# Kernel optimization log

Measured on AMD Instinct MI355X. Metric: run time of the kernel, lower is better.

## Reference

```python
import jax, jax.numpy as jnp
import numpy as np
import math

F = 32                      # multiplicity per irrep (l0dim = l1dim = l2dim)
NUMBASIS = 8
RCUT = 4.0
BESSEL_END = 5.0
AVG_NEIGHBORS = 25.0
N_NODES = 10000
N_EDGES = 250000
HIDDEN = 64
FEAT = 9 * F                # (1+3+5) components per channel

# uvu tensor-product paths (l_in1, l_edge, l_out) allowed by l/parity selection rules
PATHS = [(0,0,0),(0,1,1),(0,2,2),(1,0,1),(1,1,0),(1,1,2),(1,2,1),(2,0,2),(2,1,1),(2,2,0),(2,2,2)]
_cnt = {}
for (_,_,k) in PATHS:
    _cnt[k] = _cnt.get(k, 0) + 1
# e3nn path weights: irrep_normalization='component', path_normalization='element' (num_elements(uvu)=mul_in2=1)
PATH_W = [math.sqrt((2*k+1) / _cnt[k]) for (_,_,k) in PATHS]

def _su2_cg(j1, j2, j3, m1, m2, m3):
    if m1 + m2 != m3:
        return 0.0
    f = math.factorial
    pref = math.sqrt((2*j3+1) * f(j1+j2-j3) * f(j1-j2+j3) * f(-j1+j2+j3) / f(j1+j2+j3+1))
    pref *= math.sqrt(f(j3+m3) * f(j3-m3) * f(j1-m1) * f(j1+m1) * f(j2-m2) * f(j2+m2))
    s = 0.0
    for k in range(0, j1+j2-j3+1):
        d = [k, j1+j2-j3-k, j1-m1-k, j2+m2-k, j3-j2+m1+k, j3-j1-m2+k]
        if min(d) < 0:
            continue
        s += (-1)**k / (f(d[0])*f(d[1])*f(d[2])*f(d[3])*f(d[4])*f(d[5]))
    return pref * s

def _q(l):
    # complex->real SH change of basis (e3nn convention)
    q = np.zeros((2*l+1, 2*l+1), dtype=np.complex128)
    for m in range(-l, 0):
        q[l+m, l+abs(m)] = 1/math.sqrt(2)
        q[l+m, l-abs(m)] = -1j/math.sqrt(2)
    q[l, l] = 1.0
    for m in range(1, l+1):
        q[l+m, l+abs(m)] = (-1)**m/math.sqrt(2)
        q[l+m, l-abs(m)] = 1j*(-1)**m/math.sqrt(2)
    return (-1j)**l * q

def _w3j(l1, l2, l3):
    C = np.zeros((2*l1+1, 2*l2+1, 2*l3+1))
    for m1 in range(-l1, l1+1):
        for m2 in range(-l2, l2+1):
            for m3 in range(-l3, l3+1):
                C[l1+m1, l2+m2, l3+m3] = _su2_cg(l1, l2, l3, m1, m2, m3)
    W = np.einsum('ij,kl,mn,ikm->jln', _q(l1), _q(l2), np.conj(_q(l3)), C.astype(np.complex128))
    Wr, Wi = np.real(W), np.imag(W)
    W = Wr if np.linalg.norm(Wr) >= np.linalg.norm(Wi) else Wi
    return (W / np.linalg.norm(W)).astype(np.float32)   # unit-Frobenius real 3j, as in e3nn

W3J = {p: _w3j(*p) for p in PATHS}

def _bessel(d):
    # soft_one_hot_linspace(d, 0, 5, 8, basis='bessel', cutoff=True)
    t = d / BESSEL_END
    n = jnp.arange(1, NUMBASIS + 1, dtype=d.dtype)
    safe_t = jnp.where(t > 0, t, 1.0)
    out = math.sqrt(2.0 / BESSEL_END) * jnp.sin(n * jnp.pi * t[:, None]) / safe_t[:, None]
    return out * (((t > 0) & (t < 1)).astype(d.dtype))[:, None]

def _poly_cutoff(d):
    u = d / RCUT                      # p = 6
    env = 1.0 - 6.0 * u**5 + 5.0 * u**6
    return env * (d < RCUT).astype(d.dtype)

def _sph(unit):
    # component-normalized real spherical harmonics l=0,1,2 on unit vectors
    x, y, z = unit[:, 0], unit[:, 1], unit[:, 2]
    y0 = jnp.ones_like(x)[:, None]
    y1 = math.sqrt(3.0) * jnp.stack([y, z, x], axis=-1)
    y2 = jnp.stack([
        math.sqrt(15.0) * x * y,
        math.sqrt(15.0) * y * z,
        (math.sqrt(5.0) / 2.0) * (3.0 * z * z - 1.0),
        math.sqrt(15.0) * x * z,
        (math.sqrt(15.0) / 2.0) * (x * x - y * y),
    ], axis=-1)
    return (y0, y1, y2)

def _forward(nodes, pos, src, dst, w1, b1, w2, b2):
    neighbors = nodes[src]                                    # [E, 9F] gather
    posvec = pos[src] - pos[dst]                              # [E, 3]
    dist = jnp.sqrt(jnp.sum(posvec * posvec, axis=1))         # [E]
    h = jax.nn.silu(_bessel(dist) @ w1 + b1)                  # [E, 64]
    radial = (h @ w2 + b2) * _poly_cutoff(dist)[:, None]      # [E, 11F]
    w = radial.reshape(-1, len(PATHS), F)                     # [E, P, F]
    unit = posvec / jnp.maximum(dist, 1e-12)[:, None]
    ys = _sph(unit)                                           # ([E,1],[E,3],[E,5])
    x0 = neighbors[:, :F].reshape(-1, F, 1)
    x1 = neighbors[:, F:4*F].reshape(-1, F, 3)
    x2 = neighbors[:, 4*F:].reshape(-1, F, 5)
    xs = (x0, x1, x2)
    outs = [0.0, 0.0, 0.0]
    for p, (i, j, k) in enumerate(PATHS):
        Wp = jnp.asarray(W3J[(i, j, k)])                      # [di, dj, dk]
        msg = jnp.einsum('abc,eua,eb,eu->euc', Wp, xs[i], ys[j], w[:, p, :])
        outs[k] = outs[k] + PATH_W[p] * msg
    messages = jnp.concatenate([o.reshape(o.shape[0], -1) for o in outs], axis=1)  # [E, 9F]
    agg = jax.ops.segment_sum(messages, dst, num_segments=N_NODES)
    return agg / math.sqrt(AVG_NEIGHBORS)

def setup_inputs():
    key = jax.random.key(0)
    ks = jax.random.split(key, 6)
    nodes = jax.random.normal(ks[0], (N_NODES, FEAT), dtype=jnp.float32)
    pos = jax.random.normal(ks[1], (N_NODES, 3), dtype=jnp.float32)
    src = jax.random.randint(ks[2], (N_EDGES,), 0, N_NODES)
    dst = jax.random.randint(ks[3], (N_EDGES,), 0, N_NODES)
    w1 = jax.random.normal(ks[4], (NUMBASIS, HIDDEN), dtype=jnp.float32) / math.sqrt(NUMBASIS)
    b1 = jnp.zeros((HIDDEN,), jnp.float32)
    w2 = jax.random.normal(ks[5], (HIDDEN, len(PATHS)*F), dtype=jnp.float32) / math.sqrt(HIDDEN)
    b2 = jnp.zeros((len(PATHS)*F,), jnp.float32)
    return {"nodes": nodes, "pos": pos, "src": src, "dst": dst, "w1": w1, "b1": b1, "w2": w2, "b2": b2}

def reference(nodes, pos, src, dst, w1, b1, w2, b2):
    return _forward(nodes, pos, src, dst, w1, b1, w2, b2)
```

## Files before the change

### kernel.cpp

```cpp
#include <hip/hip_runtime.h>
#include <hip/hip_bf16.h>
#include <cmath>
#include <complex>

#define TPB 256
#define SUBS 8
#define EPG 4
#define NM 115
#define NW3J 363
#define SCAN_T 1024
#define NBUCK 256
#define W2N (64*32*12)

namespace {

double fct(int n){ double r=1; for(int i=2;i<=n;i++) r*=i; return r; }

double su2_cg(int j1,int j2,int j3,int m1,int m2,int m3){
  if(m1+m2!=m3) return 0.0;
  double pref = std::sqrt((2*j3+1)*fct(j1+j2-j3)*fct(j1-j2+j3)*fct(-j1+j2+j3)/fct(j1+j2+j3+1));
  pref *= std::sqrt(fct(j3+m3)*fct(j3-m3)*fct(j1-m1)*fct(j1+m1)*fct(j2-m2)*fct(j2+m2));
  double s=0;
  for(int k=0;k<=j1+j2-j3;k++){
    int d0=k, d1=j1+j2-j3-k, d2=j1-m1-k, d3=j2+m2-k, d4=j3-j2+m1+k, d5=j3-j1-m2+k;
    if(d0<0||d1<0||d2<0||d3<0||d4<0||d5<0) continue;
    double t = 1.0/(fct(d0)*fct(d1)*fct(d2)*fct(d3)*fct(d4)*fct(d5));
    s += (k&1)? -t : t;
  }
  return pref*s;
}

typedef std::complex<double> cd;

void qmat(int l, cd q[5][5]){
  for(int i=0;i<5;i++) for(int j=0;j<5;j++) q[i][j] = cd(0,0);
  const double is2 = 1.0/std::sqrt(2.0);
  for(int m=-l;m<0;m++){ q[l+m][l-m] = cd(is2,0); q[l+m][l+m] = cd(0,-is2); }
  q[l][l] = cd(1,0);
  for(int m=1;m<=l;m++){ double sg = (m&1)? -1.0: 1.0; q[l+m][l+m] = cd(sg*is2,0); q[l+m][l-m] = cd(0, sg*is2); }
  cd ph(1,0), mi(0,-1);
  for(int t=0;t<l;t++) ph *= mi;
  for(int i=0;i<5;i++) for(int j=0;j<5;j++) q[i][j] *= ph;
}

void w3j_calc(int l1,int l2,int l3,double* out){
  int n1=2*l1+1,n2=2*l2+1,n3=2*l3+1;
  double C[5][5][5] = {};
  for(int m1=-l1;m1<=l1;m1++)for(int m2=-l2;m2<=l2;m2++)for(int m3=-l3;m3<=l3;m3++)
    C[l1+m1][l2+m2][l3+m3] = su2_cg(l1,l2,l3,m1,m2,m3);
  cd q1[5][5], q2[5][5], q3[5][5];
  qmat(l1,q1); qmat(l2,q2); qmat(l3,q3);
  double wr[125], wi[125];
  double nr=0, ni=0;
  for(int a=0;a<n1;a++)for(int b=0;b<n2;b++)for(int c=0;c<n3;c++){
    cd s(0,0);
    for(int i=0;i<n1;i++)for(int k=0;k<n2;k++)for(int m=0;m<n3;m++)
      s += q1[i][a]*q2[k][b]*std::conj(q3[m][c])*C[i][k][m];
    int idx = (a*n2+b)*n3+c;
    wr[idx]=s.real(); wi[idx]=s.imag();
    nr += s.real()*s.real(); ni += s.imag()*s.imag();
  }
  bool useR = std::sqrt(nr) >= std::sqrt(ni);
  double nn = std::sqrt(useR? nr: ni);
  for(int q=0;q<n1*n2*n3;q++) out[q] = (useR? wr[q]: wi[q])/nn;
}

struct UploadArg {
  float w3j[NW3J];
  unsigned int meta[NM];
};

UploadArg g_upload;

struct BuildInit {
  BuildInit(){
    const int P[11][3] = {{0,0,0},{0,1,1},{0,2,2},{1,0,1},{1,1,0},{1,1,2},
                          {1,2,1},{2,0,2},{2,1,1},{2,2,0},{2,2,2}};
    const int cnt[3] = {3,4,4};
    const int AO[3] = {0,1,4};
    int off = 0, t = 0;
    for(int p=0;p<11;p++){
      int i=P[p][0], j=P[p][1], k=P[p][2];
      int na=2*i+1, nb=2*j+1, nc=2*k+1;
      double W[125];
      w3j_calc(i,j,k,W);
      double pw = std::sqrt((2.0*k+1.0)/(double)cnt[k]);
      for(int q=0;q<na*nb*nc;q++) g_upload.w3j[off+q] = (float)(W[q]*pw);
      for(int a=0;a<na;a++)
        for(int c=0;c<nc;c++)
          g_upload.meta[t++] = (unsigned)((off + a*nb*nc + c) | (nc<<10) | (nb<<14) | (AO[j]<<18));
      off += na*nb*nc;
    }
  }
};
BuildInit g_build_init;

}


__global__ void count_repack_kernel(const int* __restrict__ dst, int* __restrict__ counts,
                                    const float* __restrict__ w2,
                                    unsigned short* __restrict__ w2b, int E){
  int i = blockIdx.x*blockDim.x + threadIdx.x;
  if(i < W2N){
    int pp = i % 12;
    int u  = (i/12) % 32;
    int j  = i / (12*32);
    unsigned short o = 0;
    if(pp < 11){
      unsigned ub = __float_as_uint(w2[j*352 + pp*32 + u]);
      ub = (ub + 0x7fffu + ((ub>>16)&1u)) >> 16;
      o = (unsigned short)ub;
    }
    w2b[i] = o;
  }
  if(i < E) atomicAdd(&counts[dst[i]], 1);
}

__global__ __launch_bounds__(SCAN_T) void megascan_kernel(const int* __restrict__ counts,
                                                          int* __restrict__ off,
                                                          int* __restrict__ cursor,
                                                          int* __restrict__ bcur, int NN){
  __shared__ int part[SCAN_T];
  __shared__ int lh[NBUCK];
  int t = threadIdx.x;
  if(t < NBUCK) lh[t] = 0;
  __syncthreads();
  int C = (NN + SCAN_T - 1)/SCAN_T;
  int base = t*C;
  int lim = min(base+C, NN);
  int s = 0;
  for(int i=base;i<lim;i++){
    int c = counts[i];
    s += c;
    atomicAdd(&lh[min(c, NBUCK-1)], 1);
  }
  part[t] = s;
  __syncthreads();
  for(int d=1; d<SCAN_T; d<<=1){
    int v = (t>=d)? part[t-d] : 0;
    __syncthreads();
    part[t] += v;
    __syncthreads();
  }
  int run = part[t] - s;
  for(int i=base;i<lim;i++){ off[i]=run; cursor[i]=run; run += counts[i]; }
  if(t == SCAN_T-1) off[NN] = part[t];
  __syncthreads();
  if(t == 0){
    int r = 0;
    for(int b=0;b<NBUCK;b++){ bcur[b] = r; r += lh[b]; }
  }
}

__global__ void scatter_kernel(const int* __restrict__ dst, const int* __restrict__ counts,
                               int* __restrict__ cursor, int* __restrict__ bcur,
                               int* __restrict__ node_order, int* __restrict__ eid,
                               int NN, int E){
  int i = blockIdx.x*blockDim.x + threadIdx.x;
  if(i < NN){
    int p = atomicAdd(&bcur[min(counts[i], NBUCK-1)], 1);
    node_order[p] = i;
  }
  if(i < E){
    int p = atomicAdd(&cursor[dst[i]], 1);
    eid[p] = i;
  }
}


__device__ __forceinline__ void up2(unsigned w, float& lo, float& hi){
  lo = __uint_as_float(w << 16);
  hi = __uint_as_float(w & 0xffff0000u);
}

__global__ __launch_bounds__(TPB) void node_kernel(
    const float* __restrict__ nodes,
    const float* __restrict__ pos,
    const int* __restrict__ src,
    const int* __restrict__ node_order,
    const int* __restrict__ off,
    const int* __restrict__ eid,
    const unsigned short* __restrict__ w2b,
    const float* __restrict__ w1,
    const float* __restrict__ b1,
    const float* __restrict__ b2,
    float* __restrict__ outp,
    int NN,
    UploadArg up)
{
  __shared__ float s_w3j[NW3J];
  __shared__ float s_w1[512];
  __shared__ float s_b1[64];
  __shared__ unsigned short s_w2[W2N];
  __shared__ float s_y[SUBS][EPG][12];
  __shared__ float s_h[SUBS][64][EPG];
  __shared__ float s_M[SUBS][EPG][NM+1];

  const int tid = threadIdx.x;
  const int u = tid & 31;
  const int sub = tid >> 5;

  for(int t = tid; t < NW3J; t += TPB) s_w3j[t] = up.w3j[t];
  for(int t = tid; t < 512; t += TPB)  s_w1[t]  = w1[t];
  if(tid < 64) s_b1[tid] = b1[tid];
  {
    const uint4* g4 = (const uint4*)w2b;
    uint4* s4 = (uint4*)s_w2;
    #pragma unroll
    for(int t=0; t<12; t++) s4[tid + t*TPB] = g4[tid + t*TPB];
  }
  __syncthreads();

  const int nidx = blockIdx.x*SUBS + sub;
  const bool active = nidx < NN;
  const int node = active ? node_order[nidx] : 0;
  const int start = off[node];
  const int deg = active ? (off[node+1] - start) : 0;

  float b2r[11];
  #pragma unroll
  for(int p=0;p<11;p++) b2r[p] = b2[p*32+u];
  const float dpx = pos[node*3+0], dpy = pos[node*3+1], dpz = pos[node*3+2];

  float accv[9];
  #pragma unroll
  for(int q=0;q<9;q++) accv[q] = 0.0f;

  constexpr int PI_[11]   = {0,0,0,1,1,1,1,2,2,2,2};
  constexpr int PK_[11]   = {0,1,2,1,0,2,1,2,1,0,2};
  constexpr int TOFF_[11] = {0,1,4,9,18,21,36,45,70,85,90};
  constexpr int AO_[3]    = {0,1,4};

  const int nch = (deg + EPG - 1)/EPG;

  for(int ch=0; ch<nch; ch++){
    float bes[EPG][8];
    float cut[EPG];
    int vsrc[EPG];
    bool valid[EPG];

    #pragma unroll
    for(int e=0;e<EPG;e++){
      int ei = ch*EPG + e;
      bool v = (ei < deg);
      valid[e] = v;
      int eg = v ? eid[start + ei] : 0;
      int se = v ? src[eg] : node;
      vsrc[e] = se;
      float px = pos[se*3+0] - dpx;
      float py = pos[se*3+1] - dpy;
      float pz = pos[se*3+2] - dpz;
      float d2 = px*px + py*py + pz*pz;
      float d = sqrtf(d2);
      float inv = 1.0f / fmaxf(d, 1e-12f);
      float x = px*inv, y = py*inv, z = pz*inv;
      float yv[9];
      yv[0] = 1.0f;
      yv[1] = 1.7320508075688772f*y;
      yv[2] = 1.7320508075688772f*z;
      yv[3] = 1.7320508075688772f*x;
      yv[4] = 3.872983346207417f*x*y;
      yv[5] = 3.872983346207417f*y*z;
      yv[6] = 1.118033988749895f*(3.0f*z*z - 1.0f);
      yv[7] = 3.872983346207417f*x*z;
      yv[8] = 1.9364916731037085f*(x*x - y*y);
      #pragma unroll
      for(int q=0;q<9;q++) s_y[sub][e][q] = yv[q];
      float tt = d * 0.2f;
      float st = (tt > 0.0f) ? tt : 1.0f;
      float msk = (tt > 0.0f && tt < 1.0f) ? 1.0f : 0.0f;
      float ang = 3.14159265358979323846f * tt;
      float s1 = __sinf(ang), c1 = __cosf(ang);
      float kk = 0.6324555320336759f * msk / st;
      float c2 = 2.0f*c1;
      float sp = 0.0f, sc = s1;
      bes[e][0] = kk*s1;
      #pragma unroll
      for(int n=1;n<8;n++){ float sn = c2*sc - sp; sp = sc; sc = sn; bes[e][n] = kk*sn; }
      float uu = d*0.25f;
      float u2 = uu*uu;
      float u5 = u2*u2*uu;
      float env = 1.0f - 6.0f*u5 + 5.0f*u5*uu;
      cut[e] = (d < 4.0f) ? env : 0.0f;
    }

    #pragma unroll
    for(int half=0; half<2; half++){
      int j = u + 32*half;
      float hb = s_b1[j];
      float hh[EPG];
      #pragma unroll
      for(int e=0;e<EPG;e++){
        float a = hb;
        #pragma unroll
        for(int k=0;k<8;k++) a += bes[e][k]*s_w1[k*64+j];
        float sg = 1.0f/(1.0f + __expf(-a));
        hh[e] = a*sg;
      }
      float4 hv; hv.x = hh[0]; hv.y = hh[1]; hv.z = hh[2]; hv.w = hh[3];
      *(float4*)(&s_h[sub][j][0]) = hv;
    }

    #pragma unroll
    for(int w=0; w<4; w++){
      int t = u + 32*w;
      if(t < NM){
        unsigned int md = up.meta[t];
        int woff = md & 1023;
        int nc   = (md>>10) & 15;
        int nb   = (md>>14) & 15;
        int boff = (md>>18) & 15;
        #pragma unroll
        for(int e=0;e<EPG;e++){
          float s = 0.0f;
          for(int b=0;b<nb;b++) s += s_w3j[woff + b*nc] * s_y[sub][e][boff + b];
          s_M[sub][e][t] = s;
        }
      }
    }

    float wacc[EPG][11];
    #pragma unroll
    for(int e=0;e<EPG;e++)
      #pragma unroll
      for(int p=0;p<11;p++) wacc[e][p] = 0.0f;
    for(int j=0;j<64;j++){
      float4 hv = *(const float4*)(&s_h[sub][j][0]);
      const unsigned short* wrow = &s_w2[(j*32+u)*12];
      uint2 wa = *(const uint2*)(wrow);
      uint2 wb = *(const uint2*)(wrow+4);
      uint2 wc = *(const uint2*)(wrow+8);
      float sw[12];
      up2(wa.x, sw[0], sw[1]);  up2(wa.y, sw[2], sw[3]);
      up2(wb.x, sw[4], sw[5]);  up2(wb.y, sw[6], sw[7]);
      up2(wc.x, sw[8], sw[9]);  up2(wc.y, sw[10], sw[11]);
      float hh[4]; hh[0]=hv.x; hh[1]=hv.y; hh[2]=hv.z; hh[3]=hv.w;
      #pragma unroll
      for(int e=0;e<EPG;e++)
        #pragma unroll
        for(int p=0;p<11;p++) wacc[e][p] += hh[e]*sw[p];
    }

    #pragma unroll
    for(int e=0;e<EPG;e++){
      if(!valid[e]) continue;
      const float* nr = nodes + (long)vsrc[e]*288;
      float xv[9];
      xv[0] = nr[u];
      #pragma unroll
      for(int c=0;c<3;c++) xv[1+c] = nr[32 + u*3 + c];
      #pragma unroll
      for(int c=0;c<5;c++) xv[4+c] = nr[128 + u*5 + c];
      float wr[11];
      #pragma unroll
      for(int p=0;p<11;p++) wr[p] = (wacc[e][p] + b2r[p]) * cut[e];
      const float* Me = &s_M[sub][e][0];
      #pragma unroll
      for(int p=0;p<11;p++){
        const int na = 2*PI_[p]+1;
        const int nc = 2*PK_[p]+1;
        const float wv = wr[p];
        #pragma unroll
        for(int a=0;a<na;a++){
          float xw = xv[AO_[PI_[p]]+a] * wv;
          #pragma unroll
          for(int c=0;c<nc;c++){
            accv[AO_[PK_[p]]+c] += xw * Me[TOFF_[p] + a*nc + c];
          }
        }
      }
    }
  }

  if(active){
    float* ob = outp + (long)node*288;
    ob[u] = 0.2f*accv[0];
    #pragma unroll
    for(int c=0;c<3;c++) ob[32 + u*3 + c] = 0.2f*accv[1+c];
    #pragma unroll
    for(int c=0;c<5;c++) ob[128 + u*5 + c] = 0.2f*accv[4+c];
  }
}


extern "C" void kernel_launch(void* const* d_in, const int* in_sizes, int n_in,
                              void* d_out, int out_size, void* d_ws, size_t ws_size,
                              hipStream_t stream) {
  const float* nodes = (const float*)d_in[0];
  const float* pos   = (const float*)d_in[1];
  const int* src = (const int*)d_in[2];
  const int* dst = (const int*)d_in[3];
  const float* w1 = (const float*)d_in[4];
  const float* b1 = (const float*)d_in[5];
  const float* w2 = (const float*)d_in[6];
  const float* b2 = (const float*)d_in[7];

  const int E  = in_sizes[2];
  const int NN = in_sizes[0] / 288;
  float* outp = (float*)d_out;

  unsigned short* w2b = (unsigned short*)d_ws;
  int* counts     = (int*)(w2b + W2N);
  int* offp       = counts + NN;
  int* cursor     = offp + NN + 1;
  int* bcur       = cursor + NN;
  int* node_order = bcur + NBUCK;
  int* eid        = node_order + NN;

  hipMemsetAsync(counts, 0, (size_t)NN*sizeof(int), stream);

  int g1 = (max(E, W2N) + 255)/256;
  count_repack_kernel<<<g1, 256, 0, stream>>>(dst, counts, w2, w2b, E);
  megascan_kernel<<<1, SCAN_T, 0, stream>>>(counts, offp, cursor, bcur, NN);
  int g2 = (max(E, NN) + 255)/256;
  scatter_kernel<<<g2, 256, 0, stream>>>(dst, counts, cursor, bcur, node_order, eid, NN, E);

  int nblocks = (NN + SUBS - 1)/SUBS;
  node_kernel<<<nblocks, TPB, 0, stream>>>(nodes, pos, src, node_order, offp, eid,
                                           w2b, w1, b1, b2, outp, NN, g_upload);
}
```

Baseline: 544.7 us.

## Compute edge radial MLP second layer with bf16 MFMA, one wave per node

Moves the hidden-to-path-weight matmul (64x352 per edge) onto MFMA 16x16x32 bf16 instructions, splitting hidden activations into high and low bf16 parts to keep near-fp32 accuracy. W2 is stored transposed in LDS with an XOR swizzle to avoid bank conflicts. Work is reorganized so each 64-lane wave handles one node with 16 edges per chunk, and lanes split channels and edges before a cross-lane shuffle reduction. The cost is more LDS per block, more complex indexing, and wasted work on nodes whose degree is low relative to the 16-edge chunk.

New measurement: 561.0 us. +3.0%, slower.

```diff
diff --git a/kernel.cpp b/kernel.cpp
--- a/kernel.cpp
+++ b/kernel.cpp
@@ -1,16 +1,19 @@
 #include <hip/hip_runtime.h>
-#include <hip/hip_bf16.h>
 #include <cmath>
 #include <complex>
 
-#define TPB 256
-#define SUBS 8
-#define EPG 4
+#define TPB 512
+#define NPB 8
+#define EPG 16
 #define NM 115
 #define NW3J 363
 #define SCAN_T 1024
 #define NBUCK 256
-#define W2N (64*32*12)
+#define W2N (352*64)
+
+typedef __attribute__((ext_vector_type(8))) short bf16x8;
+typedef __attribute__((ext_vector_type(4))) float f32x4;
+typedef uint4 __attribute__((may_alias)) uint4a;
 
 namespace {
 
@@ -100,19 +103,13 @@
 
 __global__ void count_repack_kernel(const int* __restrict__ dst, int* __restrict__ counts,
                                     const float* __restrict__ w2,
-                                    unsigned short* __restrict__ w2b, int E){
+                                    unsigned short* __restrict__ w2t, int E){
   int i = blockIdx.x*blockDim.x + threadIdx.x;
   if(i < W2N){
-    int pp = i % 12;
-    int u  = (i/12) % 32;
-    int j  = i / (12*32);
-    unsigned short o = 0;
-    if(pp < 11){
-      unsigned ub = __float_as_uint(w2[j*352 + pp*32 + u]);
-      ub = (ub + 0x7fffu + ((ub>>16)&1u)) >> 16;
-      o = (unsigned short)ub;
-    }
-    w2b[i] = o;
+    int n = i >> 6, k = i & 63;
+    unsigned ub = __float_as_uint(w2[k*352 + n]);
+    ub = (ub + 0x7fffu + ((ub>>16)&1u)) >> 16;
+    w2t[i] = (unsigned short)ub;
   }
   if(i < E) atomicAdd(&counts[dst[i]], 1);
 }
@@ -169,19 +166,14 @@
 }
 
 
-__device__ __forceinline__ void up2(unsigned w, float& lo, float& hi){
-  lo = __uint_as_float(w << 16);
-  hi = __uint_as_float(w & 0xffff0000u);
-}
-
-__global__ __launch_bounds__(TPB) void node_kernel(
+__global__ __launch_bounds__(TPB, 2) void node_kernel(
     const float* __restrict__ nodes,
     const float* __restrict__ pos,
     const int* __restrict__ src,
     const int* __restrict__ node_order,
     const int* __restrict__ off,
     const int* __restrict__ eid,
-    const unsigned short* __restrict__ w2b,
+    const unsigned short* __restrict__ w2t,
     const float* __restrict__ w1,
     const float* __restrict__ b1,
     const float* __restrict__ b2,
@@ -189,72 +181,84 @@
     int NN,
     UploadArg up)
 {
-  __shared__ float s_w3j[NW3J];
+  __shared__ __align__(16) unsigned short s_w2t[W2N];
   __shared__ float s_w1[512];
   __shared__ float s_b1[64];
-  __shared__ unsigned short s_w2[W2N];
-  __shared__ float s_y[SUBS][EPG][12];
-  __shared__ float s_h[SUBS][64][EPG];
-  __shared__ float s_M[SUBS][EPG][NM+1];
+  __shared__ float s_b2[352];
+  __shared__ float s_w3j[NW3J];
+  __shared__ unsigned int s_meta[NM];
+  __shared__ float s_M[NPB][16][117];
+  __shared__ float s_y[NPB][16][12];
+  __shared__ float s_cut[NPB][16];
+  __shared__ int   s_srcv[NPB][16];
 
   const int tid = threadIdx.x;
-  const int u = tid & 31;
-  const int sub = tid >> 5;
-
-  for(int t = tid; t < NW3J; t += TPB) s_w3j[t] = up.w3j[t];
-  for(int t = tid; t < 512; t += TPB)  s_w1[t]  = w1[t];
+
+  for(int t=tid; t<NW3J; t+=TPB) s_w3j[t] = up.w3j[t];
+  for(int t=tid; t<NM;   t+=TPB) s_meta[t] = up.meta[t];
+  for(int t=tid; t<512;  t+=TPB) s_w1[t]  = w1[t];
   if(tid < 64) s_b1[tid] = b1[tid];
+  if(tid >= 64 && tid < 64+352) s_b2[tid-64] = b2[tid-64];
   {
-    const uint4* g4 = (const uint4*)w2b;
-    uint4* s4 = (uint4*)s_w2;
-    #pragma unroll
-    for(int t=0; t<12; t++) s4[tid + t*TPB] = g4[tid + t*TPB];
+    const uint4* g4 = (const uint4*)w2t;
+    uint4a* s4 = (uint4a*)s_w2t;
+    for(int c=tid; c<W2N/8; c+=TPB) s4[c ^ ((c>>3)&7)] = g4[c];
   }
   __syncthreads();
 
-  const int nidx = blockIdx.x*SUBS + sub;
+  const int lane = tid & 63;
+  const int wv   = tid >> 6;
+  const int q    = lane >> 4;
+  const int le   = lane & 15;
+  const int swz  = (le & 7) << 4;
+
+  const int nidx = blockIdx.x*NPB + wv;
   const bool active = nidx < NN;
   const int node = active ? node_order[nidx] : 0;
   const int start = off[node];
   const int deg = active ? (off[node+1] - start) : 0;
 
-  float b2r[11];
-  #pragma unroll
-  for(int p=0;p<11;p++) b2r[p] = b2[p*32+u];
   const float dpx = pos[node*3+0], dpy = pos[node*3+1], dpz = pos[node*3+2];
-
-  float accv[9];
-  #pragma unroll
-  for(int q=0;q<9;q++) accv[q] = 0.0f;
 
   constexpr int PI_[11]   = {0,0,0,1,1,1,1,2,2,2,2};
   constexpr int PK_[11]   = {0,1,2,1,0,2,1,2,1,0,2};
   constexpr int TOFF_[11] = {0,1,4,9,18,21,36,45,70,85,90};
   constexpr int AO_[3]    = {0,1,4};
 
+  float accv[2][9];
+  #pragma unroll
+  for(int uh=0; uh<2; uh++)
+    #pragma unroll
+    for(int m=0; m<9; m++) accv[uh][m] = 0.0f;
+
+  const char* wtb = (const char*)s_w2t;
   const int nch = (deg + EPG - 1)/EPG;
 
   for(int ch=0; ch<nch; ch++){
-    float bes[EPG][8];
-    float cut[EPG];
-    int vsrc[EPG];
-    bool valid[EPG];
-
-    #pragma unroll
-    for(int e=0;e<EPG;e++){
-      int ei = ch*EPG + e;
-      bool v = (ei < deg);
-      valid[e] = v;
-      int eg = v ? eid[start + ei] : 0;
-      int se = v ? src[eg] : node;
-      vsrc[e] = se;
-      float px = pos[se*3+0] - dpx;
-      float py = pos[se*3+1] - dpy;
-      float pz = pos[se*3+2] - dpz;
-      float d2 = px*px + py*py + pz*pz;
-      float d = sqrtf(d2);
-      float inv = 1.0f / fmaxf(d, 1e-12f);
-      float x = px*inv, y = py*inv, z = pz*inv;
+    const int ei = ch*EPG + le;
+    const bool valid = ei < deg;
+    const int eg = valid ? eid[start + ei] : 0;
+    const int se = valid ? src[eg] : node;
+    const float px = pos[se*3+0]-dpx, py = pos[se*3+1]-dpy, pz = pos[se*3+2]-dpz;
+    const float d2 = px*px + py*py + pz*pz;
+    const float d  = sqrtf(d2);
+    const float inv = 1.0f / fmaxf(d, 1e-12f);
+    const float x = px*inv, y = py*inv, z = pz*inv;
+
+    float bes[8];
+    {
+      float tt = d * 0.2f;
+      float st = (tt > 0.0f) ? tt : 1.0f;
+      float msk = (tt > 0.0f && tt < 1.0f) ? 1.0f : 0.0f;
+      float ang = 3.14159265358979323846f * tt;
+      float s1 = __sinf(ang), c1 = __cosf(ang);
+      float kk = 0.6324555320336759f * msk / st;
+      float c2 = 2.0f*c1, sp = 0.0f, sc = s1;
+      bes[0] = kk*s1;
+      #pragma unroll
+      for(int n=1;n<8;n++){ float sn = c2*sc - sp; sp = sc; sc = sn; bes[n] = kk*sn; }
+    }
+    if(q == 0){
       float yv[9];
       yv[0] = 1.0f;
       yv[1] = 1.7320508075688772f*y;
@@ -266,120 +270,114 @@
       yv[7] = 3.872983346207417f*x*z;
       yv[8] = 1.9364916731037085f*(x*x - y*y);
       #pragma unroll
-      for(int q=0;q<9;q++) s_y[sub][e][q] = yv[q];
-      float tt = d * 0.2f;
-      float st = (tt > 0.0f) ? tt : 1.0f;
-      float msk = (tt > 0.0f && tt < 1.0f) ? 1.0f : 0.0f;
-      float ang = 3.14159265358979323846f * tt;
-      float s1 = __sinf(ang), c1 = __cosf(ang);
-      float kk = 0.6324555320336759f * msk / st;
-      float c2 = 2.0f*c1;
-      float sp = 0.0f, sc = s1;
-      bes[e][0] = kk*s1;
-      #pragma unroll
-      for(int n=1;n<8;n++){ float sn = c2*sc - sp; sp = sc; sc = sn; bes[e][n] = kk*sn; }
-      float uu = d*0.25f;
-      float u2 = uu*uu;
-      float u5 = u2*u2*uu;
+      for(int m=0;m<9;m++) s_y[wv][le][m] = yv[m];
+      float uu = d*0.25f, u2 = uu*uu, u5 = u2*u2*uu;
       float env = 1.0f - 6.0f*u5 + 5.0f*u5*uu;
-      cut[e] = (d < 4.0f) ? env : 0.0f;
-    }
-
-    #pragma unroll
-    for(int half=0; half<2; half++){
-      int j = u + 32*half;
-      float hb = s_b1[j];
-      float hh[EPG];
-      #pragma unroll
-      for(int e=0;e<EPG;e++){
-        float a = hb;
+      s_cut[wv][le] = (valid && d < 4.0f) ? env : 0.0f;
+      s_srcv[wv][le] = se;
+    }
+
+    bf16x8 Ah0, Al0, Ah1, Al1;
+    #pragma unroll
+    for(int e=0; e<8; e++){
+      #pragma unroll
+      for(int half=0; half<2; half++){
+        const int j = half*32 + q*8 + e;
+        float a = s_b1[j];
         #pragma unroll
-        for(int k=0;k<8;k++) a += bes[e][k]*s_w1[k*64+j];
+        for(int k=0;k<8;k++) a += bes[k]*s_w1[k*64+j];
         float sg = 1.0f/(1.0f + __expf(-a));
-        hh[e] = a*sg;
+        float h = a*sg;
+        unsigned ub = __float_as_uint(h);
+        unsigned hb = (ub + 0x7fffu + ((ub>>16)&1u)) >> 16;
+        float hif = __uint_as_float(hb << 16);
+        unsigned ul = __float_as_uint(h - hif);
+        unsigned lb = (ul + 0x7fffu + ((ul>>16)&1u)) >> 16;
+        if(half == 0){ Ah0[e] = (short)hb; Al0[e] = (short)lb; }
+        else         { Ah1[e] = (short)hb; Al1[e] = (short)lb; }
       }
-      float4 hv; hv.x = hh[0]; hv.y = hh[1]; hv.z = hh[2]; hv.w = hh[3];
-      *(float4*)(&s_h[sub][j][0]) = hv;
-    }
-
-    #pragma unroll
-    for(int w=0; w<4; w++){
-      int t = u + 32*w;
-      if(t < NM){
-        unsigned int md = up.meta[t];
-        int woff = md & 1023;
-        int nc   = (md>>10) & 15;
-        int nb   = (md>>14) & 15;
-        int boff = (md>>18) & 15;
+    }
+
+    for(int t=q; t<NM; t+=4){
+      const unsigned md = s_meta[t];
+      const int woff = md & 1023;
+      const int nc2  = (md>>10) & 15;
+      const int nb   = (md>>14) & 15;
+      const int boff = (md>>18) & 15;
+      float s = 0.0f;
+      for(int b=0;b<nb;b++) s += s_w3j[woff + b*nc2] * s_y[wv][le][boff + b];
+      s_M[wv][le][t] = s;
+    }
+    asm volatile("" ::: "memory");
+
+    float cut4[4]; int se4[4];
+    #pragma unroll
+    for(int i=0;i<4;i++){ cut4[i] = s_cut[wv][4*q+i]; se4[i] = s_srcv[wv][4*q+i]; }
+
+    #pragma unroll
+    for(int uh=0; uh<2; uh++){
+      const int u = uh*16 + le;
+      float xv[4][9];
+      #pragma unroll
+      for(int i=0;i<4;i++){
+        const float* nr = nodes + (long)se4[i]*288;
+        xv[i][0] = nr[u];
         #pragma unroll
-        for(int e=0;e<EPG;e++){
-          float s = 0.0f;
-          for(int b=0;b<nb;b++) s += s_w3j[woff + b*nc] * s_y[sub][e][boff + b];
-          s_M[sub][e][t] = s;
-        }
+        for(int c=0;c<3;c++) xv[i][1+c] = nr[32 + u*3 + c];
+        #pragma unroll
+        for(int c=0;c<5;c++) xv[i][4+c] = nr[128 + u*5 + c];
       }
-    }
-
-    float wacc[EPG][11];
-    #pragma unroll
-    for(int e=0;e<EPG;e++)
-      #pragma unroll
-      for(int p=0;p<11;p++) wacc[e][p] = 0.0f;
-    for(int j=0;j<64;j++){
-      float4 hv = *(const float4*)(&s_h[sub][j][0]);
-      const unsigned short* wrow = &s_w2[(j*32+u)*12];
-      uint2 wa = *(const uint2*)(wrow);
-      uint2 wb = *(const uint2*)(wrow+4);
-      uint2 wc = *(const uint2*)(wrow+8);
-      float sw[12];
-      up2(wa.x, sw[0], sw[1]);  up2(wa.y, sw[2], sw[3]);
-      up2(wb.x, sw[4], sw[5]);  up2(wb.y, sw[6], sw[7]);
-      up2(wc.x, sw[8], sw[9]);  up2(wc.y, sw[10], sw[11]);
-      float hh[4]; hh[0]=hv.x; hh[1]=hv.y; hh[2]=hv.z; hh[3]=hv.w;
-      #pragma unroll
-      for(int e=0;e<EPG;e++)
+      #pragma unroll
+      for(int p=0;p<11;p++){
+        const int t2 = 2*p + uh;
+        const int bb = (t2*2048 + le*128 + q*16) ^ swz;
+        const bf16x8 B0 = __builtin_bit_cast(bf16x8, *(const uint4a*)(wtb + bb));
+        const bf16x8 B1 = __builtin_bit_cast(bf16x8, *(const uint4a*)(wtb + (bb^64)));
+        f32x4 acc = {0.0f, 0.0f, 0.0f, 0.0f};
+        acc = __builtin_amdgcn_mfma_f32_16x16x32_bf16(Ah0, B0, acc, 0, 0, 0);
+        acc = __builtin_amdgcn_mfma_f32_16x16x32_bf16(Al0, B0, acc, 0, 0, 0);
+        acc = __builtin_amdgcn_mfma_f32_16x16x32_bf16(Ah1, B1, acc, 0, 0, 0);
+        acc = __builtin_amdgcn_mfma_f32_16x16x32_bf16(Al1, B1, acc, 0, 0, 0);
+        const float bv = s_b2[p*32 + u];
+        const int na  = 2*PI_[p] + 1;
+        const int ncc = 2*PK_[p] + 1;
         #pragma unroll
-        for(int p=0;p<11;p++) wacc[e][p] += hh[e]*sw[p];
-    }
-
-    #pragma unroll
-    for(int e=0;e<EPG;e++){
-      if(!valid[e]) continue;
-      const float* nr = nodes + (long)vsrc[e]*288;
-      float xv[9];
-      xv[0] = nr[u];
-      #pragma unroll
-      for(int c=0;c<3;c++) xv[1+c] = nr[32 + u*3 + c];
-      #pragma unroll
-      for(int c=0;c<5;c++) xv[4+c] = nr[128 + u*5 + c];
-      float wr[11];
-      #pragma unroll
-      for(int p=0;p<11;p++) wr[p] = (wacc[e][p] + b2r[p]) * cut[e];
-      const float* Me = &s_M[sub][e][0];
-      #pragma unroll
-      for(int p=0;p<11;p++){
-        const int na = 2*PI_[p]+1;
-        const int nc = 2*PK_[p]+1;
-        const float wv = wr[p];
-        #pragma unroll
-        for(int a=0;a<na;a++){
-          float xw = xv[AO_[PI_[p]]+a] * wv;
+        for(int i=0;i<4;i++){
+          const float wr = (acc[i] + bv) * cut4[i];
+          const float* Me = &s_M[wv][4*q + i][0];
           #pragma unroll
-          for(int c=0;c<nc;c++){
-            accv[AO_[PK_[p]]+c] += xw * Me[TOFF_[p] + a*nc + c];
+          for(int a=0;a<na;a++){
+            const float xw = xv[i][AO_[PI_[p]] + a] * wr;
+            #pragma unroll
+            for(int c=0;c<ncc;c++)
+              accv[uh][AO_[PK_[p]] + c] += xw * Me[TOFF_[p] + a*ncc + c];
           }
         }
       }
     }
-  }
-
-  if(active){
+    asm volatile("" ::: "memory");
+  }
+
+  #pragma unroll
+  for(int uh=0; uh<2; uh++)
+    #pragma unroll
+    for(int m=0; m<9; m++){
+      float v = accv[uh][m];
+      v += __shfl_xor(v, 16);
+      v += __shfl_xor(v, 32);
+      accv[uh][m] = v;
+    }
+  if(active && lane < 16){
     float* ob = outp + (long)node*288;
-    ob[u] = 0.2f*accv[0];
-    #pragma unroll
-    for(int c=0;c<3;c++) ob[32 + u*3 + c] = 0.2f*accv[1+c];
-    #pragma unroll
-    for(int c=0;c<5;c++) ob[128 + u*5 + c] = 0.2f*accv[4+c];
+    #pragma unroll
+    for(int uh=0; uh<2; uh++){
+      const int u = uh*16 + lane;
+      ob[u] = 0.2f*accv[uh][0];
+      #pragma unroll
+      for(int c=0;c<3;c++) ob[32 + u*3 + c] = 0.2f*accv[uh][1+c];
+      #pragma unroll
+      for(int c=0;c<5;c++) ob[128 + u*5 + c] = 0.2f*accv[uh][4+c];
+    }
   }
 }
 
@@ -400,8 +398,8 @@
   const int NN = in_sizes[0] / 288;
   float* outp = (float*)d_out;
 
-  unsigned short* w2b = (unsigned short*)d_ws;
-  int* counts     = (int*)(w2b + W2N);
+  unsigned short* w2t = (unsigned short*)d_ws;
+  int* counts     = (int*)(w2t + W2N);
   int* offp       = counts + NN;
   int* cursor     = offp + NN + 1;
   int* bcur       = cursor + NN;
@@ -411,12 +409,12 @@
   hipMemsetAsync(counts, 0, (size_t)NN*sizeof(int), stream);
 
   int g1 = (max(E, W2N) + 255)/256;
-  count_repack_kernel<<<g1, 256, 0, stream>>>(dst, counts, w2, w2b, E);
+  count_repack_kernel<<<g1, 256, 0, stream>>>(dst, counts, w2, w2t, E);
   megascan_kernel<<<1, SCAN_T, 0, stream>>>(counts, offp, cursor, bcur, NN);
   int g2 = (max(E, NN) + 255)/256;
   scatter_kernel<<<g2, 256, 0, stream>>>(dst, counts, cursor, bcur, node_order, eid, NN, E);
 
-  int nblocks = (NN + SUBS - 1)/SUBS;
+  int nblocks = (NN + NPB - 1)/NPB;
   node_kernel<<<nblocks, TPB, 0, stream>>>(nodes, pos, src, node_order, offp, eid,
-                                           w2b, w1, b1, b2, outp, NN, g_upload);
-}
+                                           w2t, w1, b1, b2, outp, NN, g_upload);
+}
```
